# Performance work log

Hardware: AMD Instinct MI355X
Metric: run time of the kernel (lower is better)

## Reference

```python
import jax, jax.numpy as jnp
import numpy as np

P, B, S = 128, 32, 64          # num_packet, batch, bytes per packet
E = 50                          # byte/packet embedding size (hard-coded in module)
Hb = 128; Hp = 128; Po = 128   # byte hidden, packet hidden, packet output
V = 256 * 256; NCLS = 11


def setup_inputs() -> dict:
    key = jax.random.key(0)
    ks = jax.random.split(key, 12)
    rn = lambda k, shp, s: (jax.random.normal(k, shp, jnp.float32) * s)
    return {
        'flow': jax.random.randint(ks[0], (P, B, S), 0, V),
        'emb': rn(ks[1], (V, E), 0.1),
        'byte_Wih': rn(ks[2], (2, 3 * Hb, E), 1.0 / np.sqrt(E)),
        'byte_Whh': rn(ks[3], (2, 3 * Hb, Hb), 1.0 / np.sqrt(Hb)),
        'byte_attn_W': rn(ks[4], (E, 2 * Hb), 1.0 / np.sqrt(2 * Hb)),
        'byte_attn_b': jnp.zeros((E,), jnp.float32),
        'pkt_Wih': rn(ks[5], (2, 3 * Hp, E), 1.0 / np.sqrt(E)),
        'pkt_Whh': rn(ks[6], (2, 3 * Hp, Hp), 1.0 / np.sqrt(Hp)),
        'pkt_attn_W': rn(ks[7], (Po, 2 * Hp), 1.0 / np.sqrt(2 * Hp)),
        'pkt_attn_b': jnp.zeros((Po,), jnp.float32),
        'cls_W': rn(ks[8], (NCLS, Po), 1.0 / np.sqrt(Po)),
        'cls_b': jnp.zeros((NCLS,), jnp.float32),
        'h0_bytes': rn(ks[9], (P, 2, B, Hb), 1.0),   # per-packet random h0 (torch.randn in fwd)
        'h0_packet': rn(ks[10], (2, B, Hp), 1.0),
    }


def _gru_dir(xW, h0, Whh, H):
    # xW: (S, N, 3H) precomputed input projections; h0: (N, H). PyTorch gate order r,z,n; no bias.
    def step(h, xw):
        hW = h @ Whh.T
        r = jax.nn.sigmoid(xw[:, :H] + hW[:, :H])
        z = jax.nn.sigmoid(xw[:, H:2 * H] + hW[:, H:2 * H])
        n = jnp.tanh(xw[:, 2 * H:] + r * hW[:, 2 * H:])
        h_new = (1.0 - z) * n + z * h
        return h_new, h_new
    hT, ys = jax.lax.scan(step, h0, xW)
    return ys, hT


def bigru(x, h0, Wih, Whh, H):
    # x: (S, N, E); h0: (2, N, H) -> outputs (S, N, 2H), final hidden (2, N, H)
    xWf = jnp.einsum('sne,ge->sng', x, Wih[0])
    xWb = jnp.einsum('sne,ge->sng', x[::-1], Wih[1])
    yf, hf = _gru_dir(xWf, h0[0], Whh[0], H)
    yb, hb = _gru_dir(xWb, h0[1], Whh[1], H)
    return jnp.concatenate([yf, yb[::-1]], axis=-1), jnp.stack([hf, hb])


def reference(flow, emb, byte_Wih, byte_Whh, byte_attn_W, byte_attn_b,
              pkt_Wih, pkt_Whh, pkt_attn_W, pkt_attn_b, cls_W, cls_b,
              h0_bytes, h0_packet):
    Pn, Bn, Sn = flow.shape
    x = emb[flow]                                             # (P, B, S, E)
    # Fold packets into batch: one byte-level bi-GRU call instead of a Python loop over P.
    xs = x.transpose(2, 0, 1, 3).reshape(Sn, Pn * Bn, E)      # (S, P*B, E)
    h0b = h0_bytes.transpose(1, 0, 2, 3).reshape(2, Pn * Bn, Hb)
    y, hn = bigru(xs, h0b, byte_Wih, byte_Whh, Hb)            # y (S, P*B, 2Hb), hn (2, P*B, Hb)
    out = y.transpose(1, 0, 2).reshape(Pn, Bn, Sn, 2 * Hb)    # (P, B, S, 2Hb)
    # torch view(-1, 2Hb, 1) on each per-packet (2, B, Hb) final state == raw C-order reshape
    hn_p = hn.reshape(2, Pn, Bn, Hb).transpose(1, 0, 2, 3).reshape(Pn, Bn, 2 * Hb)
    aw = jax.nn.softmax(jnp.einsum('pbsh,pbh->pbs', out, hn_p), axis=-1)
    ctx = jnp.einsum('pbsh,pbs->pbh', out, aw)                # (P, B, 2Hb)
    enc = ctx @ byte_attn_W.T + byte_attn_b                   # (P, B, E)

    y2, hn2 = bigru(enc, h0_packet, pkt_Wih, pkt_Whh, Hp)     # (P, B, 2Hp), (2, B, Hp)
    out2 = y2.transpose(1, 0, 2)                              # (B, P, 2Hp)
    hn2v = hn2.reshape(Bn, 2 * Hp)                            # view(-1, byte_hidden*2) semantics
    aw2 = jax.nn.softmax(jnp.einsum('bph,bh->bp', out2, hn2v), axis=-1)
    ctx2 = jnp.einsum('bph,bp->bh', out2, aw2)                # (B, 2Hp)
    o = ctx2 @ pkt_attn_W.T + pkt_attn_b                      # (B, Po)
    return o @ cls_W.T + cls_b                                # (B, 11)
```

## Files before the change

### kernel.cpp

```cpp
#include <hip/hip_runtime.h>
#include <hip/hip_bf16.h>

#define PD 128
#define BD 32
#define SD 64
#define ED 50
#define HD 128
#define GD 384
#define ND 4096
#define VD 65536
#define LW 128

typedef __attribute__((ext_vector_type(8))) short bf16x8;
typedef __attribute__((ext_vector_type(4))) float f32x4;

__device__ __forceinline__ float sigm(float x) { return 1.0f / (1.0f + __expf(-x)); }
__device__ __forceinline__ float tanh_f(float x) { return 1.0f - 2.0f / (__expf(2.0f * x) + 1.0f); }

__device__ __forceinline__ unsigned short f2b(float f) {
    union { float f; unsigned u; } a; a.f = f;
    unsigned r = a.u + 0x7FFFu + ((a.u >> 16) & 1u);
    return (unsigned short)(r >> 16);
}
__device__ __forceinline__ float b2f(unsigned short h) {
    union { unsigned u; float f; } a; a.u = ((unsigned)h) << 16; return a.f;
}

union frag_u { bf16x8 v; unsigned short s[8]; };

__device__ __forceinline__ void pin_v(bf16x8& v) { asm volatile("" : "+v"(v)); }

#define MFMA(acc, a, b) acc = __builtin_amdgcn_mfma_f32_16x16x32_bf16(a, b, acc, 0, 0, 0)

__device__ __forceinline__ void block_sync_lds() {
    asm volatile("s_waitcnt lgkmcnt(0)" ::: "memory");
    __builtin_amdgcn_sched_barrier(0);
    __builtin_amdgcn_s_barrier();
    __builtin_amdgcn_sched_barrier(0);
}

__global__ void prep_all(const float* __restrict__ emb, unsigned short* __restrict__ embHi,
                         const float* __restrict__ aW, float* __restrict__ aWT,
                         const float* __restrict__ pWih, float* __restrict__ pWT) {
    int idx = blockIdx.x * 256 + threadIdx.x;
    if (idx < VD * 64) {
        int row = idx >> 6, e = idx & 63;
        float v = (e < ED) ? emb[row * ED + e] : 0.f;
        embHi[idx] = f2b(v);
    }
    if (idx < 256 * 64) {
        int c = idx >> 6, e = idx & 63;
        aWT[idx] = (e < ED) ? aW[e * 256 + c] : 0.f;
    }
    if (idx < 2 * 64 * GD) {
        int g = idx % GD, r = idx / GD;
        int d = r >> 6, e = r & 63;
        pWT[idx] = (e < ED) ? pWih[((size_t)(d * GD + g)) * ED + e] : 0.f;
    }
}

__global__ __attribute__((amdgpu_flat_work_group_size(512, 512), amdgpu_waves_per_eu(2, 2)))
void byte_gru_mfma(
    const int* __restrict__ flow, const unsigned short* __restrict__ embHi,
    const float* __restrict__ Wih, const float* __restrict__ Whh,
    const float* __restrict__ h0b,
    unsigned short* __restrict__ y, float* __restrict__ hn) {
    const int dir   = blockIdx.x >> 7;
    const int chunk = blockIdx.x & 127;
    const int n0    = chunk * 32;
    const int tid   = threadIdx.x;
    const int w     = tid >> 6;
    const int lane  = tid & 63;
    const int col   = lane & 15;
    const int kq    = lane >> 4;
    const int u     = w * 16 + col;

    __shared__ unsigned short HHI[2][32 * LW];
    __shared__ unsigned short HLO[2][32 * LW];
    __shared__ int FLOWT[SD * 32];

    const int yrow = tid >> 4;
    const int yu0  = (tid & 15) * 8;
    const int ysw  = yrow * LW + (yu0 ^ ((yrow & 7) << 3));

    bf16x8 WHh[3][4], WHl[3][4], WXh[3][2], WXl[3][2];
    {
        const float* WhhD = Whh + dir * GD * HD;
        #pragma unroll
        for (int g3 = 0; g3 < 3; ++g3) {
            const float* row = WhhD + (g3 * HD + u) * HD;
            #pragma unroll
            for (int kt = 0; kt < 4; ++kt) {
                const int k0 = kt * 32 + kq * 8;
                frag_u h_, l_;
                #pragma unroll
                for (int b = 0; b < 8; ++b) {
                    float v = row[k0 + b];
                    unsigned short hi = f2b(v);
                    h_.s[b] = hi; l_.s[b] = f2b(v - b2f(hi));
                }
                WHh[g3][kt] = h_.v; WHl[g3][kt] = l_.v;
                pin_v(WHh[g3][kt]); pin_v(WHl[g3][kt]);
            }
        }
        const float* WihD = Wih + dir * GD * ED;
        #pragma unroll
        for (int g3 = 0; g3 < 3; ++g3) {
            const float* row = WihD + (g3 * HD + u) * ED;
            #pragma unroll
            for (int kx = 0; kx < 2; ++kx) {
                const int k0 = kx * 32 + kq * 8;
                frag_u h_, l_;
                #pragma unroll
                for (int b = 0; b < 8; ++b) {
                    const int e = k0 + b;
                    float v = (e < ED) ? row[e] : 0.f;
                    unsigned short hi = f2b(v);
                    h_.s[b] = hi; l_.s[b] = f2b(v - b2f(hi));
                }
                WXh[g3][kx] = h_.v; WXl[g3][kx] = l_.v;
                pin_v(WXh[g3][kx]); pin_v(WXl[g3][kx]);
            }
        }
    }

    float hreg[2][4];
    {
        const float* h0row = h0b + (size_t)((chunk * 2 + dir) * 32) * HD;
        #pragma unroll
        for (int m = 0; m < 2; ++m)
            #pragma unroll
            for (int j = 0; j < 4; ++j)
                hreg[m][j] = h0row[(m * 16 + kq * 4 + j) * HD + u];
        for (int idx = tid; idx < 32 * HD; idx += 512) {
            int seq = idx >> 7, uu = idx & 127;
            float v = h0row[idx];
            unsigned short hi = f2b(v);
            int sw = seq * LW + (uu ^ ((seq & 7) << 3));
            HHI[0][sw] = hi; HLO[0][sw] = f2b(v - b2f(hi));
        }
        for (int j = tid; j < SD * 32; j += 512) {
            int s = j >> 5, seq = j & 31;
            FLOWT[j] = flow[(n0 + seq) * SD + s];
        }
    }
    block_sync_lds();

    bf16x8 xa00, xa01, xa10, xa11;
    {
        const int s0 = dir ? (SD - 1) : 0;
        int i0 = FLOWT[s0 * 32 + col];
        int i1 = FLOWT[s0 * 32 + 16 + col];
        const bf16x8* r0 = (const bf16x8*)(embHi + (size_t)i0 * 64);
        const bf16x8* r1 = (const bf16x8*)(embHi + (size_t)i1 * 64);
        xa00 = r0[kq]; xa01 = r0[4 + kq];
        xa10 = r1[kq]; xa11 = r1[4 + kq];
    }

    int par = 0;
    for (int t = 0; t < SD; ++t) {
        const int s = dir ? (SD - 1 - t) : t;

        if (t > 0) {
            const int sp = dir ? (SD - t) : (t - 1);
            uint4 v = *(const uint4*)&HHI[par][ysw];
            *(uint4*)&y[((size_t)(sp * ND) + n0 + yrow) * 256 + dir * HD + yu0] = v;
        }

        bf16x8 xn00, xn01, xn10, xn11;
        if (t < SD - 1) {
            const int sn = dir ? (SD - 2 - t) : (t + 1);
            int i0 = FLOWT[sn * 32 + col];
            int i1 = FLOWT[sn * 32 + 16 + col];
            const bf16x8* r0 = (const bf16x8*)(embHi + (size_t)i0 * 64);
            const bf16x8* r1 = (const bf16x8*)(embHi + (size_t)i1 * 64);
            xn00 = r0[kq]; xn01 = r0[4 + kq];
            xn10 = r1[kq]; xn11 = r1[4 + kq];
        }

        f32x4 aR[2], aZ[2], aHN[2], aXN[2];
        const f32x4 zero = {0.f, 0.f, 0.f, 0.f};
        #pragma unroll
        for (int m = 0; m < 2; ++m) { aR[m] = zero; aZ[m] = zero; aHN[m] = zero; aXN[m] = zero; }

        const unsigned short* HHIp = HHI[par];
        const unsigned short* HLOp = HLO[par];
        #pragma unroll
        for (int kt = 0; kt < 4; ++kt) {
            const int off = kt * 32 + kq * 8;
            const int sw0 = col * LW + (off ^ ((col & 7) << 3));
            const int sw1 = sw0 + 16 * LW;
            bf16x8 ah0 = *(const bf16x8*)&HHIp[sw0];
            bf16x8 al0 = *(const bf16x8*)&HLOp[sw0];
            bf16x8 ah1 = *(const bf16x8*)&HHIp[sw1];
            bf16x8 al1 = *(const bf16x8*)&HLOp[sw1];
            MFMA(aR[0], ah0, WHh[0][kt]); MFMA(aR[0], al0, WHh[0][kt]); MFMA(aR[0], ah0, WHl[0][kt]);
            MFMA(aZ[0], ah0, WHh[1][kt]); MFMA(aZ[0], al0, WHh[1][kt]); MFMA(aZ[0], ah0, WHl[1][kt]);
            MFMA(aHN[0], ah0, WHh[2][kt]); MFMA(aHN[0], al0, WHh[2][kt]); MFMA(aHN[0], ah0, WHl[2][kt]);
            MFMA(aR[1], ah1, WHh[0][kt]); MFMA(aR[1], al1, WHh[0][kt]); MFMA(aR[1], ah1, WHl[0][kt]);
            MFMA(aZ[1], ah1, WHh[1][kt]); MFMA(aZ[1], al1, WHh[1][kt]); MFMA(aZ[1], ah1, WHl[1][kt]);
            MFMA(aHN[1], ah1, WHh[2][kt]); MFMA(aHN[1], al1, WHh[2][kt]); MFMA(aHN[1], ah1, WHl[2][kt]);
        }
        #pragma unroll
        for (int kx = 0; kx < 2; ++kx) {
            bf16x8 x0 = kx ? xa01 : xa00;
            bf16x8 x1 = kx ? xa11 : xa10;
            MFMA(aR[0], x0, WXh[0][kx]); MFMA(aR[0], x0, WXl[0][kx]);
            MFMA(aZ[0], x0, WXh[1][kx]); MFMA(aZ[0], x0, WXl[1][kx]);
            MFMA(aXN[0], x0, WXh[2][kx]); MFMA(aXN[0], x0, WXl[2][kx]);
            MFMA(aR[1], x1, WXh[0][kx]); MFMA(aR[1], x1, WXl[0][kx]);
            MFMA(aZ[1], x1, WXh[1][kx]); MFMA(aZ[1], x1, WXl[1][kx]);
            MFMA(aXN[1], x1, WXh[2][kx]); MFMA(aXN[1], x1, WXl[2][kx]);
        }

        unsigned short* HHIn = HHI[par ^ 1];
        unsigned short* HLOn = HLO[par ^ 1];
        #pragma unroll
        for (int m = 0; m < 2; ++m)
            #pragma unroll
            for (int j = 0; j < 4; ++j) {
                float r = sigm(aR[m][j]);
                float z = sigm(aZ[m][j]);
                float nn = tanh_f(aXN[m][j] + r * aHN[m][j]);
                float hnew = (1.f - z) * nn + z * hreg[m][j];
                hreg[m][j] = hnew;
                __hip_bfloat16 bh = __float2bfloat16(hnew);
                unsigned short hi = *(unsigned short*)&bh;
                __hip_bfloat16 bl = __float2bfloat16(hnew - b2f(hi));
                const int seq = m * 16 + kq * 4 + j;
                const int sw = seq * LW + (u ^ ((seq & 7) << 3));
                HHIn[sw] = hi;
                HLOn[sw] = *(unsigned short*)&bl;
            }
        block_sync_lds();
        xa00 = xn00; xa01 = xn01; xa10 = xn10; xa11 = xn11;
        par ^= 1;
    }
    {
        const int sl = dir ? 0 : (SD - 1);
        uint4 v = *(const uint4*)&HHI[par][ysw];
        *(uint4*)&y[((size_t)(sl * ND) + n0 + yrow) * 256 + dir * HD + yu0] = v;
    }
    #pragma unroll
    for (int m = 0; m < 2; ++m)
        #pragma unroll
        for (int j = 0; j < 4; ++j) {
            int seq = m * 16 + kq * 4 + j;
            hn[((size_t)dir * ND + n0 + seq) * HD + u] = hreg[m][j];
        }
}

__global__ __launch_bounds__(256) void byte_attn(
    const unsigned short* __restrict__ y, const float* __restrict__ hn,
    const float* __restrict__ aWT, const float* __restrict__ ab,
    const float* __restrict__ pWT, float* __restrict__ pxw) {
    const int n = blockIdx.x;
    const int p = n >> 5, irow = n & 31;
    const int tid = threadIdx.x;
    __shared__ unsigned short yl[SD][256];
    __shared__ float hnl[256];
    __shared__ float red[256];
    __shared__ float red2[256];
    __shared__ float awl[SD];
    __shared__ float ctxl[256];
    __shared__ float encl[64];

    for (int idx = tid; idx < SD * 32; idx += 256) {
        int s = idx >> 5, cc = (idx & 31) * 8;
        *(uint4*)&yl[s][cc] = *(const uint4*)&y[((s * ND) + n) * 256 + cc];
    }
    {
        int c = tid;
        int idx = irow * 256 + c;
        int d = idx >> 12, bb = (idx >> 7) & 31, uu = idx & 127;
        hnl[c] = hn[(d * ND + p * 32 + bb) * HD + uu];
    }
    __syncthreads();
    {
        int s = tid & 63, grp = tid >> 6;
        float acc = 0.f;
        for (int k = 0; k < 32; ++k) {
            int c2 = grp * 32 + ((s + k) & 31);
            unsigned pair = *(const unsigned*)&yl[s][c2 * 2];
            float2 hv = *(const float2*)&hnl[c2 * 2];
            union { unsigned u; float f; } lo, hi;
            lo.u = pair << 16; hi.u = pair & 0xFFFF0000u;
            acc += lo.f * hv.x + hi.f * hv.y;
        }
        red[grp * 64 + s] = acc;
    }
    __syncthreads();
    if (tid < 64) {
        float sc = red[tid] + red[64 + tid] + red[128 + tid] + red[192 + tid];
        float m = sc;
        #pragma unroll
        for (int o = 32; o; o >>= 1) m = fmaxf(m, __shfl_xor(m, o));
        float e = __expf(sc - m);
        float ssum = e;
        #pragma unroll
        for (int o = 32; o; o >>= 1) ssum += __shfl_xor(ssum, o);
        awl[tid] = e / ssum;
    }
    __syncthreads();
    {
        int c2 = tid & 127, sh = tid >> 7;
        float a0 = 0.f, a1 = 0.f;
        const int s0 = sh * 32;
        for (int s = s0; s < s0 + 32; ++s) {
            unsigned pair = *(const unsigned*)&yl[s][c2 * 2];
            union { unsigned u; float f; } lo, hi;
            lo.u = pair << 16; hi.u = pair & 0xFFFF0000u;
            float aw = awl[s];
            a0 += aw * lo.f; a1 += aw * hi.f;
        }
        float* dst = sh ? red2 : red;
        *(float2*)&dst[c2 * 2] = make_float2(a0, a1);
    }
    __syncthreads();
    ctxl[tid] = red[tid] + red2[tid];
    __syncthreads();
    {
        int e = tid & 63, q = tid >> 6;
        float acc = 0.f;
        for (int c = q * 64; c < q * 64 + 64; ++c) acc += ctxl[c] * aWT[c * 64 + e];
        red[q * 64 + e] = acc;
    }
    __syncthreads();
    if (tid < 64) {
        float v = red[tid] + red[64 + tid] + red[128 + tid] + red[192 + tid];
        encl[tid] = (tid < ED) ? (v + ab[tid]) : 0.f;
    }
    __syncthreads();
    {
        int fg0 = tid, fg1 = tid + 256, fg2 = tid + 512;
        int d0 = fg0 >= GD, d1 = fg1 >= GD, d2 = fg2 >= GD;
        int g0 = fg0 - d0 * GD, g1 = fg1 - d1 * GD, g2 = fg2 - d2 * GD;
        const float* wr0 = pWT + (size_t)(d0 * 64) * GD + g0;
        const float* wr1 = pWT + (size_t)(d1 * 64) * GD + g1;
        const float* wr2 = pWT + (size_t)(d2 * 64) * GD + g2;
        float a0 = 0.f, a1 = 0.f, a2 = 0.f;
        #pragma unroll 2
        for (int e = 0; e < ED; ++e) {
            float ev = encl[e];
            size_t o = (size_t)e * GD;
            a0 += ev * wr0[o]; a1 += ev * wr1[o]; a2 += ev * wr2[o];
        }
        pxw[((size_t)(d0 * PD + p) * 32 + irow) * GD + g0] = a0;
        pxw[((size_t)(d1 * PD + p) * 32 + irow) * GD + g1] = a1;
        pxw[((size_t)(d2 * PD + p) * 32 + irow) * GD + g2] = a2;
    }
}

__global__ __launch_bounds__(768, 1) void pkt_gru(
    const float* __restrict__ pxw, const float* __restrict__ Whh,
    const float* __restrict__ h0p,
    float* __restrict__ y2, float* __restrict__ hn2) {
    const int d = blockIdx.x >> 5, sq = blockIdx.x & 31;
    const int tid = threadIdx.x;
    const int g   = tid >> 1;
    const int hf  = tid & 1;
    __shared__ float hcur[HD];
    __shared__ float hwp[GD * 2];
    float w[64];
    const float* wrow = Whh + (size_t)(d * GD + g) * HD + hf * 64;
    #pragma unroll
    for (int k = 0; k < 64; ++k) w[k] = wrow[k];
    if (tid < HD) hcur[tid] = h0p[(d * 32 + sq) * HD + tid];

    float xr = 0.f, xz = 0.f, xn_ = 0.f;
    if (tid < HD) {
        const int p0 = d ? (PD - 1) : 0;
        const float* xw = pxw + (size_t)((d * PD + p0) * 32 + sq) * GD;
        xr = xw[tid]; xz = xw[HD + tid]; xn_ = xw[2 * HD + tid];
    }
    block_sync_lds();
    for (int t = 0; t < PD; ++t) {
        const int pp = d ? (PD - 1 - t) : t;
        float xrn = 0.f, xzn = 0.f, xnn = 0.f;
        if (t < PD - 1 && tid < HD) {
            const int pn = d ? (PD - 2 - t) : (t + 1);
            const float* xw = pxw + (size_t)((d * PD + pn) * 32 + sq) * GD;
            xrn = xw[tid]; xzn = xw[HD + tid]; xnn = xw[2 * HD + tid];
        }
        float a0 = 0.f, a1 = 0.f, a2 = 0.f, a3 = 0.f;
        const float* hb = &hcur[hf * 64];
        #pragma unroll
        for (int kc = 0; kc < 16; ++kc) {
            float4 h4 = *(const float4*)(hb + kc * 4);
            a0 += w[4 * kc + 0] * h4.x; a1 += w[4 * kc + 1] * h4.y;
            a2 += w[4 * kc + 2] * h4.z; a3 += w[4 * kc + 3] * h4.w;
        }
        hwp[tid] = (a0 + a1) + (a2 + a3);
        block_sync_lds();
        if (tid < HD) {
            int uu = tid;
            float2 pr = *(const float2*)&hwp[2 * uu];
            float2 pz = *(const float2*)&hwp[2 * (HD + uu)];
            float2 pn_ = *(const float2*)&hwp[2 * (2 * HD + uu)];
            float r = sigm(xr + (pr.x + pr.y));
            float z = sigm(xz + (pz.x + pz.y));
            float nn = tanh_f(xn_ + r * (pn_.x + pn_.y));
            float hnew = (1.f - z) * nn + z * hcur[uu];
            hcur[uu] = hnew;
            y2[(pp * 32 + sq) * 256 + d * HD + uu] = hnew;
        }
        block_sync_lds();
        xr = xrn; xz = xzn; xn_ = xnn;
    }
    if (tid < HD) hn2[(d * 32 + sq) * HD + tid] = hcur[tid];
}

__global__ __launch_bounds__(256) void pkt_attn_cls(
    const float* __restrict__ y2, const float* __restrict__ hn2,
    const float* __restrict__ aW, const float* __restrict__ ab,
    const float* __restrict__ cW, const float* __restrict__ cb,
    float* __restrict__ out) {
    const int b = blockIdx.x;
    const int tid = threadIdx.x;
    __shared__ float yl2[32][257];
    __shared__ float hnl[256];
    __shared__ float red[256];
    __shared__ float scl[PD];
    __shared__ float awl[PD];
    __shared__ float ctxl[256];
    __shared__ float ol[HD];
    hnl[tid] = hn2[(((b >> 4) * 32) + 2 * (b & 15) + (tid >> 7)) * HD + (tid & 127)];
    for (int ch = 0; ch < 4; ++ch) {
        __syncthreads();
        for (int idx = tid; idx < 32 * 256; idx += 256) {
            int r = idx >> 8, c = idx & 255;
            yl2[r][c] = y2[((ch * 32 + r) * 32 + b) * 256 + c];
        }
        __syncthreads();
        {
            int r = tid >> 3, seg = tid & 7;
            float acc = 0.f;
            for (int i = 0; i < 32; ++i) {
                int c = seg * 32 + ((i + seg * 4) & 31);
                acc += yl2[r][c] * hnl[c];
            }
            red[tid] = acc;
        }
        __syncthreads();
        if (tid < 32) {
            float s = 0.f;
            #pragma unroll
            for (int k = 0; k < 8; ++k) s += red[tid * 8 + k];
            scl[ch * 32 + tid] = s;
        }
    }
    __syncthreads();
    if (tid < 64) {
        float s0 = scl[tid], s1 = scl[64 + tid];
        float m = fmaxf(s0, s1);
        #pragma unroll
        for (int o = 32; o; o >>= 1) m = fmaxf(m, __shfl_xor(m, o));
        float e0 = __expf(s0 - m), e1 = __expf(s1 - m);
        float ss = e0 + e1;
        #pragma unroll
        for (int o = 32; o; o >>= 1) ss += __shfl_xor(ss, o);
        awl[tid] = e0 / ss; awl[64 + tid] = e1 / ss;
    }
    __syncthreads();
    {
        int c = tid;
        float acc = 0.f;
        for (int p2 = 0; p2 < PD; ++p2) acc += awl[p2] * y2[(p2 * 32 + b) * 256 + c];
        ctxl[c] = acc;
    }
    __syncthreads();
    {
        int h = tid >> 1, hf = tid & 1;
        const float* wr = aW + h * 256 + hf * 128;
        const float* cr = ctxl + hf * 128;
        float acc = 0.f;
        for (int c = 0; c < 128; ++c) acc += cr[c] * wr[c];
        red[hf * 128 + h] = acc;
    }
    __syncthreads();
    if (tid < HD) ol[tid] = red[tid] + red[128 + tid] + ab[tid];
    __syncthreads();
    if (tid < 11) {
        float acc = cb[tid];
        for (int h = 0; h < HD; ++h) acc += ol[h] * cW[tid * HD + h];
        out[b * 11 + tid] = acc;
    }
}

extern "C" void kernel_launch(void* const* d_in, const int* in_sizes, int n_in,
                              void* d_out, int out_size, void* d_ws, size_t ws_size,
                              hipStream_t stream) {
    const int*   flow = (const int*)d_in[0];
    const float* emb  = (const float*)d_in[1];
    const float* bWih = (const float*)d_in[2];
    const float* bWhh = (const float*)d_in[3];
    const float* baW  = (const float*)d_in[4];
    const float* bab  = (const float*)d_in[5];
    const float* pWih = (const float*)d_in[6];
    const float* pWhh = (const float*)d_in[7];
    const float* paW  = (const float*)d_in[8];
    const float* pab  = (const float*)d_in[9];
    const float* cW   = (const float*)d_in[10];
    const float* cb   = (const float*)d_in[11];
    const float* h0b  = (const float*)d_in[12];
    const float* h0p  = (const float*)d_in[13];
    float* out = (float*)d_out;

    char* ws = (char*)d_ws;
    size_t off = 0;
    unsigned short* y = (unsigned short*)(ws + off); off += (size_t)SD * ND * 256 * 2;
    float* hn    = (float*)(ws + off); off += (size_t)2 * ND * HD * 4;
    float* pxw   = (float*)(ws + off); off += (size_t)2 * PD * 32 * GD * 4;
    float* y2    = (float*)(ws + off); off += (size_t)PD * 32 * 256 * 4;
    float* hn2   = (float*)(ws + off); off += (size_t)2 * 32 * HD * 4;
    unsigned short* embHi = (unsigned short*)(ws + off); off += (size_t)VD * 64 * 2;
    float* aWT   = (float*)(ws + off); off += (size_t)256 * 64 * 4;
    float* pWT   = (float*)(ws + off); off += (size_t)2 * 64 * GD * 4;
    if (ws_size < off) return;

    prep_all<<<(VD * 64 + 255) / 256, 256, 0, stream>>>(emb, embHi, baW, aWT, pWih, pWT);
    byte_gru_mfma<<<256, 512, 0, stream>>>(flow, embHi, bWih, bWhh, h0b, y, hn);
    byte_attn<<<ND, 256, 0, stream>>>(y, hn, aWT, bab, pWT, pxw);
    pkt_gru<<<64, 768, 0, stream>>>(pxw, pWhh, h0p, y2, hn2);
    pkt_attn_cls<<<32, 256, 0, stream>>>(y2, hn2, paW, pab, cW, cb, out);
}
```

Before: 456.6 us.

## Split byte attention projections into batched per-packet kernel reusing weights

The byte attention kernel now only writes the context vectors to global memory. A new enc_pxw kernel runs one block per packet, computing the 50-wide encoding for 32 rows at once and holding the packet input-projection weights in registers across rows, so weight loads are amortized instead of repeated per row. Separately, the packet attention weight is transposed in the prep kernel so its matvec reads coalesced. This adds one kernel launch and a global round trip for the context vectors.

After: 610.6 us. 33.7% more time.

```diff
diff --git a/kernel.cpp b/kernel.cpp
--- a/kernel.cpp
+++ b/kernel.cpp
@@ -41,7 +41,8 @@
 
 __global__ void prep_all(const float* __restrict__ emb, unsigned short* __restrict__ embHi,
                          const float* __restrict__ aW, float* __restrict__ aWT,
-                         const float* __restrict__ pWih, float* __restrict__ pWT) {
+                         const float* __restrict__ pWih, float* __restrict__ pWT,
+                         const float* __restrict__ paW, float* __restrict__ paWT) {
     int idx = blockIdx.x * 256 + threadIdx.x;
     if (idx < VD * 64) {
         int row = idx >> 6, e = idx & 63;
@@ -56,6 +57,10 @@
         int g = idx % GD, r = idx / GD;
         int d = r >> 6, e = r & 63;
         pWT[idx] = (e < ED) ? pWih[((size_t)(d * GD + g)) * ED + e] : 0.f;
+    }
+    if (idx < 256 * HD) {
+        int c = idx >> 7, h = idx & 127;
+        paWT[idx] = paW[h * 256 + c];
     }
 }
 
@@ -252,8 +257,7 @@
 
 __global__ __launch_bounds__(256) void byte_attn(
     const unsigned short* __restrict__ y, const float* __restrict__ hn,
-    const float* __restrict__ aWT, const float* __restrict__ ab,
-    const float* __restrict__ pWT, float* __restrict__ pxw) {
+    float* __restrict__ ctxg) {
     const int n = blockIdx.x;
     const int p = n >> 5, irow = n & 31;
     const int tid = threadIdx.x;
@@ -262,8 +266,6 @@
     __shared__ float red[256];
     __shared__ float red2[256];
     __shared__ float awl[SD];
-    __shared__ float ctxl[256];
-    __shared__ float encl[64];
 
     for (int idx = tid; idx < SD * 32; idx += 256) {
         int s = idx >> 5, cc = (idx & 31) * 8;
@@ -317,37 +319,53 @@
         *(float2*)&dst[c2 * 2] = make_float2(a0, a1);
     }
     __syncthreads();
-    ctxl[tid] = red[tid] + red2[tid];
-    __syncthreads();
-    {
-        int e = tid & 63, q = tid >> 6;
-        float acc = 0.f;
-        for (int c = q * 64; c < q * 64 + 64; ++c) acc += ctxl[c] * aWT[c * 64 + e];
-        red[q * 64 + e] = acc;
-    }
-    __syncthreads();
-    if (tid < 64) {
-        float v = red[tid] + red[64 + tid] + red[128 + tid] + red[192 + tid];
-        encl[tid] = (tid < ED) ? (v + ab[tid]) : 0.f;
-    }
-    __syncthreads();
-    {
-        int fg0 = tid, fg1 = tid + 256, fg2 = tid + 512;
-        int d0 = fg0 >= GD, d1 = fg1 >= GD, d2 = fg2 >= GD;
-        int g0 = fg0 - d0 * GD, g1 = fg1 - d1 * GD, g2 = fg2 - d2 * GD;
-        const float* wr0 = pWT + (size_t)(d0 * 64) * GD + g0;
-        const float* wr1 = pWT + (size_t)(d1 * 64) * GD + g1;
-        const float* wr2 = pWT + (size_t)(d2 * 64) * GD + g2;
-        float a0 = 0.f, a1 = 0.f, a2 = 0.f;
+    ctxg[(size_t)n * 256 + tid] = red[tid] + red2[tid];
+}
+
+__global__ __launch_bounds__(768) void enc_pxw(
+    const float* __restrict__ ctxg, const float* __restrict__ aWT,
+    const float* __restrict__ ab, const float* __restrict__ pWT,
+    float* __restrict__ pxw) {
+    const int p = blockIdx.x;
+    const int tid = threadIdx.x;
+    __shared__ float ctxl[32][257];
+    __shared__ float encl[32][52];
+
+    for (int idx = tid; idx < 32 * 256; idx += 768) {
+        int r = idx >> 8, c = idx & 255;
+        ctxl[r][c] = ctxg[(size_t)(p * 32 + r) * 256 + c];
+    }
+    __syncthreads();
+    if (tid < 512) {
+        int e = tid & 63, rg = tid >> 6;
+        float a0 = 0.f, a1 = 0.f, a2 = 0.f, a3 = 0.f;
+        for (int c = 0; c < 256; ++c) {
+            float wv = aWT[c * 64 + e];
+            a0 += ctxl[rg * 4 + 0][c] * wv;
+            a1 += ctxl[rg * 4 + 1][c] * wv;
+            a2 += ctxl[rg * 4 + 2][c] * wv;
+            a3 += ctxl[rg * 4 + 3][c] * wv;
+        }
+        if (e < ED) {
+            float bb = ab[e];
+            encl[rg * 4 + 0][e] = a0 + bb;
+            encl[rg * 4 + 1][e] = a1 + bb;
+            encl[rg * 4 + 2][e] = a2 + bb;
+            encl[rg * 4 + 3][e] = a3 + bb;
+        }
+    }
+    __syncthreads();
+    {
+        int d = tid >= GD, g = tid - d * GD;
+        float wreg[ED];
         #pragma unroll 2
-        for (int e = 0; e < ED; ++e) {
-            float ev = encl[e];
-            size_t o = (size_t)e * GD;
-            a0 += ev * wr0[o]; a1 += ev * wr1[o]; a2 += ev * wr2[o];
-        }
-        pxw[((size_t)(d0 * PD + p) * 32 + irow) * GD + g0] = a0;
-        pxw[((size_t)(d1 * PD + p) * 32 + irow) * GD + g1] = a1;
-        pxw[((size_t)(d2 * PD + p) * 32 + irow) * GD + g2] = a2;
+        for (int e = 0; e < ED; ++e) wreg[e] = pWT[((size_t)(d * 64 + e)) * GD + g];
+        for (int irow = 0; irow < 32; ++irow) {
+            float acc = 0.f;
+            #pragma unroll 2
+            for (int e = 0; e < ED; ++e) acc += encl[irow][e] * wreg[e];
+            pxw[((size_t)(d * PD + p) * 32 + irow) * GD + g] = acc;
+        }
     }
 }
 
@@ -412,7 +430,7 @@
 
 __global__ __launch_bounds__(256) void pkt_attn_cls(
     const float* __restrict__ y2, const float* __restrict__ hn2,
-    const float* __restrict__ aW, const float* __restrict__ ab,
+    const float* __restrict__ paWT, const float* __restrict__ ab,
     const float* __restrict__ cW, const float* __restrict__ cb,
     float* __restrict__ out) {
     const int b = blockIdx.x;
@@ -470,11 +488,9 @@
     }
     __syncthreads();
     {
-        int h = tid >> 1, hf = tid & 1;
-        const float* wr = aW + h * 256 + hf * 128;
-        const float* cr = ctxl + hf * 128;
+        int h = tid & 127, hf = tid >> 7;
         float acc = 0.f;
-        for (int c = 0; c < 128; ++c) acc += cr[c] * wr[c];
+        for (int c = hf * 128; c < hf * 128 + 128; ++c) acc += ctxl[c] * paWT[c * 128 + h];
         red[hf * 128 + h] = acc;
     }
     __syncthreads();
@@ -510,17 +526,20 @@
     size_t off = 0;
     unsigned short* y = (unsigned short*)(ws + off); off += (size_t)SD * ND * 256 * 2;
     float* hn    = (float*)(ws + off); off += (size_t)2 * ND * HD * 4;
+    float* ctxg  = (float*)(ws + off); off += (size_t)ND * 256 * 4;
     float* pxw   = (float*)(ws + off); off += (size_t)2 * PD * 32 * GD * 4;
     float* y2    = (float*)(ws + off); off += (size_t)PD * 32 * 256 * 4;
     float* hn2   = (float*)(ws + off); off += (size_t)2 * 32 * HD * 4;
     unsigned short* embHi = (unsigned short*)(ws + off); off += (size_t)VD * 64 * 2;
     float* aWT   = (float*)(ws + off); off += (size_t)256 * 64 * 4;
     float* pWT   = (float*)(ws + off); off += (size_t)2 * 64 * GD * 4;
+    float* paWT  = (float*)(ws + off); off += (size_t)256 * HD * 4;
     if (ws_size < off) return;
 
-    prep_all<<<(VD * 64 + 255) / 256, 256, 0, stream>>>(emb, embHi, baW, aWT, pWih, pWT);
+    prep_all<<<(VD * 64 + 255) / 256, 256, 0, stream>>>(emb, embHi, baW, aWT, pWih, pWT, paW, paWT);
     byte_gru_mfma<<<256, 512, 0, stream>>>(flow, embHi, bWih, bWhh, h0b, y, hn);
-    byte_attn<<<ND, 256, 0, stream>>>(y, hn, aWT, bab, pWT, pxw);
+    byte_attn<<<ND, 256, 0, stream>>>(y, hn, ctxg);
+    enc_pxw<<<PD, 768, 0, stream>>>(ctxg, aWT, bab, pWT, pxw);
     pkt_gru<<<64, 768, 0, stream>>>(pxw, pWhh, h0p, y2, hn2);
-    pkt_attn_cls<<<32, 256, 0, stream>>>(y2, hn2, paW, pab, cW, cb, out);
-}
+    pkt_attn_cls<<<32, 256, 0, stream>>>(y2, hn2, paWT, pab, cW, cb, out);
+}
```
